# Kernel optimization log

Hardware: AMD Instinct MI355X
Metric: run time of the kernel (lower is better)

## Reference

```python
import jax, jax.numpy as jnp
import numpy as np

B = 16384
QD = 2048   # query_dim
KD = 1024   # key_dim
HID = 1024  # hidden_dim = min(QD, KD)
NH = 16     # num_heads
HD = HID // NH  # head_dim = 64
LN_EPS = 1e-5


def _ln(x, w, b):
    m = jnp.mean(x, axis=-1, keepdims=True)
    v = jnp.mean((x - m) ** 2, axis=-1, keepdims=True)
    return (x - m) * jax.lax.rsqrt(v + LN_EPS) * w + b


def _lin(x, W, b):
    return x @ W.T + b


def setup_inputs() -> dict:
    key = jax.random.key(0)
    ks = jax.random.split(key, 12)
    p = lambda k, shape: jax.random.normal(k, shape, jnp.float32) * 0.02
    return dict(
        query_features=jax.random.normal(ks[0], (B, QD), jnp.float32),
        key_features=jax.random.normal(ks[1], (B, KD), jnp.float32),
        Wq=p(ks[2], (HID, QD)), bq=jnp.zeros((HID,), jnp.float32),
        ln_q_w=jnp.ones((HID,), jnp.float32), ln_q_b=jnp.zeros((HID,), jnp.float32),
        Wk=p(ks[3], (HID, KD)), bk=jnp.zeros((HID,), jnp.float32),
        ln_k_w=jnp.ones((HID,), jnp.float32), ln_k_b=jnp.zeros((HID,), jnp.float32),
        Wvq=p(ks[4], (HID, QD)), bvq=jnp.zeros((HID,), jnp.float32),
        Wvk=p(ks[5], (HID, KD)), bvk=jnp.zeros((HID,), jnp.float32),
        Wo=p(ks[6], (QD, HID)), bo=jnp.zeros((QD,), jnp.float32),
        ln_o_w=jnp.ones((QD,), jnp.float32), ln_o_b=jnp.zeros((QD,), jnp.float32),
        Wg1=p(ks[7], (HID, QD + KD)), bg1=jnp.zeros((HID,), jnp.float32),
        Wg2=p(ks[8], (1, HID)), bg2=jnp.zeros((1,), jnp.float32),
        Wc1=p(ks[9], (HID, QD + KD)), bc1=jnp.zeros((HID,), jnp.float32),
        Wc2=p(ks[10], (1, HID)), bc2=jnp.zeros((1,), jnp.float32),
    )


def reference(query_features, key_features,
              Wq, bq, ln_q_w, ln_q_b,
              Wk, bk, ln_k_w, ln_k_b,
              Wvq, bvq, Wvk, bvk,
              Wo, bo, ln_o_w, ln_o_b,
              Wg1, bg1, Wg2, bg2,
              Wc1, bc1, Wc2, bc2):
    b = query_features.shape[0]
    q = _ln(_lin(query_features, Wq, bq), ln_q_w, ln_q_b)      # [B, HID]
    k = _ln(_lin(key_features, Wk, bk), ln_k_w, ln_k_b)        # [B, HID]
    v_q = _lin(query_features, Wvq, bvq)  # computed in torch but unused
    v_k = _lin(key_features, Wvk, bvk)    # [B, HID]
    q = q.reshape(b, NH, HD)
    k = k.reshape(b, NH, HD)
    v_k = v_k.reshape(b, NH, HD)
    # NOTE: attention mixes over the HEAD axis (j == num_heads), per original einsum
    scores = jnp.einsum('bhd,bjd->bhj', q, k) / np.sqrt(HD).astype(np.float32)
    attn = jax.nn.softmax(scores, axis=-1)  # dropout p effectively 0 / eval mode
    attended = jnp.einsum('bhj,bjd->bhd', attn, v_k).reshape(b, HID)
    output = _ln(_lin(attended, Wo, bo), ln_o_w, ln_o_b)       # [B, QD]
    combined = jnp.concatenate([query_features, key_features], axis=1)  # [B, QD+KD]
    gate = jax.nn.sigmoid(_lin(jax.nn.gelu(_lin(combined, Wg1, bg1), approximate=False), Wg2, bg2))
    chem = jax.nn.sigmoid(_lin(jax.nn.gelu(_lin(combined, Wc1, bc1), approximate=False), Wc2, bc2))
    effective_gate = gate * chem  # [B, 1]
    return query_features + effective_gate * output
```

## Files before the change

kernel.cpp:

```cpp
#include <hip/hip_runtime.h>
#include <stdint.h>

#define QD 2048
#define KD 1024
#define HID 1024
#define NH 16
#define HD 64
#define CMBD 3072

typedef float  f32x4   __attribute__((ext_vector_type(4)));
typedef short  short8  __attribute__((ext_vector_type(8)));
typedef short  short4v __attribute__((ext_vector_type(4)));
typedef float  float4v __attribute__((ext_vector_type(4)));

__device__ inline float bf2f(short s) {
  unsigned u = ((unsigned)(unsigned short)s) << 16;
  return __builtin_bit_cast(float, u);
}
__device__ inline short f2bf(float f) {
  unsigned u = __builtin_bit_cast(unsigned, f);
  u = u + 0x7fff + ((u >> 16) & 1);
  return (short)(u >> 16);
}

__global__ void cvt_inputs(const float* __restrict__ qf, const float* __restrict__ kf,
                           short* __restrict__ cmb, int rows2) {
  const int b = blockIdx.x, t = threadIdx.x;
  if (b < rows2) {
    const int i = b * 256 + t;
    const int row = i >> 9, c4 = i & 511;
    float4v v = *(const float4v*)(qf + (size_t)row * QD + c4 * 4);
    short4v o;
    o[0] = f2bf(v[0]); o[1] = f2bf(v[1]); o[2] = f2bf(v[2]); o[3] = f2bf(v[3]);
    *(short4v*)(cmb + (size_t)row * CMBD + c4 * 4) = o;
  } else {
    const int i = (b - rows2) * 256 + t;
    const int row = i >> 8, c4 = i & 255;
    float4v v = *(const float4v*)(kf + (size_t)row * KD + c4 * 4);
    short4v o;
    o[0] = f2bf(v[0]); o[1] = f2bf(v[1]); o[2] = f2bf(v[2]); o[3] = f2bf(v[3]);
    *(short4v*)(cmb + (size_t)row * CMBD + QD + c4 * 4) = o;
  }
}

struct WSeg { const float* s; short* d; int blkEnd; };
__global__ void cvt_weights(WSeg s0, WSeg s1, WSeg s2, WSeg s3, WSeg s4, WSeg s5) {
  int b = blockIdx.x;
  WSeg seg; int base;
  if      (b < s0.blkEnd) { seg = s0; base = 0; }
  else if (b < s1.blkEnd) { seg = s1; base = s0.blkEnd; }
  else if (b < s2.blkEnd) { seg = s2; base = s1.blkEnd; }
  else if (b < s3.blkEnd) { seg = s3; base = s2.blkEnd; }
  else if (b < s4.blkEnd) { seg = s4; base = s3.blkEnd; }
  else                    { seg = s5; base = s4.blkEnd; }
  const size_t i = ((size_t)(b - base) * 256 + threadIdx.x) * 4;
  float4v v = *(const float4v*)(seg.s + i);
  short4v o;
  o[0] = f2bf(v[0]); o[1] = f2bf(v[1]); o[2] = f2bf(v[2]); o[3] = f2bf(v[3]);
  *(short4v*)(seg.d + i) = o;
}

#define EPI_NONE 0
#define EPI_GATE 2

typedef const __attribute__((address_space(1))) void gvoid_t;
typedef __attribute__((address_space(3))) void lvoid_t;

#define WAIT_VM(n)  asm volatile("s_waitcnt vmcnt(" #n ")" ::: "memory")

#define APAN(b, kp) (((b) * 2 + (kp)) * 8192)
#define BPAN(b, kp) (32768 + ((b) * 2 + (kp)) * 8192)

#define PHASE_MID                                        \
  __builtin_amdgcn_s_barrier();                          \
  asm volatile("s_waitcnt lgkmcnt(0)" ::: "memory");     \
  __builtin_amdgcn_s_setprio(1);

#define PHASE_END                                        \
  __builtin_amdgcn_s_setprio(0);                         \
  __builtin_amdgcn_s_barrier();

template<int EPI>
__global__ __launch_bounds__(512, 2)
void gemm256(const short* __restrict__ A, size_t lda,
             const short* __restrict__ W,
             const float* __restrict__ bias,
             short* __restrict__ C, int N, int K,
             const float* __restrict__ w2, float* __restrict__ egp, int rowsTot) {
  extern __shared__ short ls[];
  const int tid  = threadIdx.x;
  const int lane = tid & 63;
  const int wave = tid >> 6;
  const int wm = wave >> 2, wn = wave & 3;
  const int fr = lane & 15, kq4 = lane >> 4;

  const int nwg = gridDim.x * gridDim.y;
  const int lin = blockIdx.y * gridDim.x + blockIdx.x;
  const int cpx = nwg >> 3;
  const int nid = (lin & 7) * cpx + (lin >> 3);
  const int bx = nid % gridDim.x, by = nid / gridDim.x;
  const size_t rowBase = (size_t)by * 256;
  const size_t colBase = (size_t)bx * 256;

  const int NTT = K >> 6;

  f32x4 acc[8][4];
#pragma unroll
  for (int mi = 0; mi < 8; mi++)
#pragma unroll
    for (int ni = 0; ni < 4; ni++) acc[mi][ni] = (f32x4){0.f, 0.f, 0.f, 0.f};

  const int frsw = (kq4 ^ ((fr >> 1) & 3)) * 8;

  const int grow  = tid >> 2;
  const int slotx = (tid & 3) ^ ((tid >> 3) & 3);
  const short* gAlo = A + (rowBase + grow) * lda + slotx * 8;
  const short* gAhi = gAlo + (size_t)128 * lda;
  const short* gBlo = W + (colBase + grow) * (size_t)K + slotx * 8;
  const short* gBhi = gBlo + (size_t)128 * K;
  short* const sdst = ls + tid * 8;

  auto STG_A = [&](int panOff, int kcol) {
    __builtin_amdgcn_global_load_lds((gvoid_t*)(gAlo + kcol), (lvoid_t*)(sdst + panOff),        16, 0, 0);
    __builtin_amdgcn_global_load_lds((gvoid_t*)(gAhi + kcol), (lvoid_t*)(sdst + panOff + 4096), 16, 0, 0);
  };
  auto STG_B = [&](int panOff, int kcol) {
    __builtin_amdgcn_global_load_lds((gvoid_t*)(gBlo + kcol), (lvoid_t*)(sdst + panOff),        16, 0, 0);
    __builtin_amdgcn_global_load_lds((gvoid_t*)(gBhi + kcol), (lvoid_t*)(sdst + panOff + 4096), 16, 0, 0);
  };

  STG_A(APAN(0, 0), 0);  STG_A(APAN(0, 1), 32);
  STG_B(BPAN(0, 0), 0);  STG_B(BPAN(0, 1), 32);
  STG_B(BPAN(1, 0), 64); STG_B(BPAN(1, 1), 96);
  WAIT_VM(4);
  __builtin_amdgcn_s_barrier();

  short8 fa0[8], fa1[8], fb0[4], fb1[4];

  for (int t = 0; t < NTT; t += 2) {
    const bool more = (t + 2 < NTT);
    const int kA1 = (t + 1) * 64;
    const int kE2 = (t + 2) * 64;
    const int kO3 = (t + 3) * 64;

#pragma unroll
    for (int m = 0; m < 4; m++) {
      const int r = (wm * 128 + m * 16 + fr) * 32 + frsw;
      fa0[m * 2 + 0] = *(const short8*)(ls + APAN(0, 0) + r);
      fa0[m * 2 + 1] = *(const short8*)(ls + APAN(0, 1) + r);
    }
#pragma unroll
    for (int n = 0; n < 2; n++) {
      const int r = (wn * 64 + n * 16 + fr) * 32 + frsw;
      fb0[n * 2 + 0] = *(const short8*)(ls + BPAN(0, 0) + r);
      fb0[n * 2 + 1] = *(const short8*)(ls + BPAN(0, 1) + r);
    }
    STG_A(APAN(1, 0), kA1);
    PHASE_MID
#pragma unroll
    for (int m = 0; m < 4; m++)
#pragma unroll
      for (int n = 0; n < 2; n++) {
        acc[m][n] = __builtin_amdgcn_mfma_f32_16x16x32_bf16(fa0[m*2+0], fb0[n*2+0], acc[m][n], 0, 0, 0);
        acc[m][n] = __builtin_amdgcn_mfma_f32_16x16x32_bf16(fa0[m*2+1], fb0[n*2+1], acc[m][n], 0, 0, 0);
      }
    PHASE_END

#pragma unroll
    for (int n = 0; n < 2; n++) {
      const int r = (wn * 64 + (n + 2) * 16 + fr) * 32 + frsw;
      fb1[n * 2 + 0] = *(const short8*)(ls + BPAN(0, 0) + r);
      fb1[n * 2 + 1] = *(const short8*)(ls + BPAN(0, 1) + r);
    }
    STG_A(APAN(1, 1), kA1 + 32);
    PHASE_MID
#pragma unroll
    for (int m = 0; m < 4; m++)
#pragma unroll
      for (int n = 0; n < 2; n++) {
        acc[m][n+2] = __builtin_amdgcn_mfma_f32_16x16x32_bf16(fa0[m*2+0], fb1[n*2+0], acc[m][n+2], 0, 0, 0);
        acc[m][n+2] = __builtin_amdgcn_mfma_f32_16x16x32_bf16(fa0[m*2+1], fb1[n*2+1], acc[m][n+2], 0, 0, 0);
      }
    PHASE_END

#pragma unroll
    for (int m = 0; m < 4; m++) {
      const int r = (wm * 128 + (m + 4) * 16 + fr) * 32 + frsw;
      fa1[m * 2 + 0] = *(const short8*)(ls + APAN(0, 0) + r);
      fa1[m * 2 + 1] = *(const short8*)(ls + APAN(0, 1) + r);
    }
    if (more) STG_B(BPAN(0, 0), kE2);
    PHASE_MID
#pragma unroll
    for (int m = 0; m < 4; m++)
#pragma unroll
      for (int n = 0; n < 2; n++) {
        acc[m+4][n] = __builtin_amdgcn_mfma_f32_16x16x32_bf16(fa1[m*2+0], fb0[n*2+0], acc[m+4][n], 0, 0, 0);
        acc[m+4][n] = __builtin_amdgcn_mfma_f32_16x16x32_bf16(fa1[m*2+1], fb0[n*2+1], acc[m+4][n], 0, 0, 0);
      }
    PHASE_END

    if (more) STG_B(BPAN(0, 1), kE2 + 32);
    PHASE_MID
#pragma unroll
    for (int m = 0; m < 4; m++)
#pragma unroll
      for (int n = 0; n < 2; n++) {
        acc[m+4][n+2] = __builtin_amdgcn_mfma_f32_16x16x32_bf16(fa1[m*2+0], fb1[n*2+0], acc[m+4][n+2], 0, 0, 0);
        acc[m+4][n+2] = __builtin_amdgcn_mfma_f32_16x16x32_bf16(fa1[m*2+1], fb1[n*2+1], acc[m+4][n+2], 0, 0, 0);
      }
    __builtin_amdgcn_s_setprio(0);
    if (more) { WAIT_VM(4); } else { WAIT_VM(0); }
    __builtin_amdgcn_s_barrier();

#pragma unroll
    for (int m = 0; m < 4; m++) {
      const int r = (wm * 128 + m * 16 + fr) * 32 + frsw;
      fa0[m * 2 + 0] = *(const short8*)(ls + APAN(1, 0) + r);
      fa0[m * 2 + 1] = *(const short8*)(ls + APAN(1, 1) + r);
    }
#pragma unroll
    for (int n = 0; n < 2; n++) {
      const int r = (wn * 64 + n * 16 + fr) * 32 + frsw;
      fb0[n * 2 + 0] = *(const short8*)(ls + BPAN(1, 0) + r);
      fb0[n * 2 + 1] = *(const short8*)(ls + BPAN(1, 1) + r);
    }
    if (more) STG_A(APAN(0, 0), kE2);
    PHASE_MID
#pragma unroll
    for (int m = 0; m < 4; m++)
#pragma unroll
      for (int n = 0; n < 2; n++) {
        acc[m][n] = __builtin_amdgcn_mfma_f32_16x16x32_bf16(fa0[m*2+0], fb0[n*2+0], acc[m][n], 0, 0, 0);
        acc[m][n] = __builtin_amdgcn_mfma_f32_16x16x32_bf16(fa0[m*2+1], fb0[n*2+1], acc[m][n], 0, 0, 0);
      }
    PHASE_END

#pragma unroll
    for (int n = 0; n < 2; n++) {
      const int r = (wn * 64 + (n + 2) * 16 + fr) * 32 + frsw;
      fb1[n * 2 + 0] = *(const short8*)(ls + BPAN(1, 0) + r);
      fb1[n * 2 + 1] = *(const short8*)(ls + BPAN(1, 1) + r);
    }
    if (more) STG_A(APAN(0, 1), kE2 + 32);
    PHASE_MID
#pragma unroll
    for (int m = 0; m < 4; m++)
#pragma unroll
      for (int n = 0; n < 2; n++) {
        acc[m][n+2] = __builtin_amdgcn_mfma_f32_16x16x32_bf16(fa0[m*2+0], fb1[n*2+0], acc[m][n+2], 0, 0, 0);
        acc[m][n+2] = __builtin_amdgcn_mfma_f32_16x16x32_bf16(fa0[m*2+1], fb1[n*2+1], acc[m][n+2], 0, 0, 0);
      }
    PHASE_END

#pragma unroll
    for (int m = 0; m < 4; m++) {
      const int r = (wm * 128 + (m + 4) * 16 + fr) * 32 + frsw;
      fa1[m * 2 + 0] = *(const short8*)(ls + APAN(1, 0) + r);
      fa1[m * 2 + 1] = *(const short8*)(ls + APAN(1, 1) + r);
    }
    if (more) STG_B(BPAN(1, 0), kO3);
    PHASE_MID
#pragma unroll
    for (int m = 0; m < 4; m++)
#pragma unroll
      for (int n = 0; n < 2; n++) {
        acc[m+4][n] = __builtin_amdgcn_mfma_f32_16x16x32_bf16(fa1[m*2+0], fb0[n*2+0], acc[m+4][n], 0, 0, 0);
        acc[m+4][n] = __builtin_amdgcn_mfma_f32_16x16x32_bf16(fa1[m*2+1], fb0[n*2+1], acc[m+4][n], 0, 0, 0);
      }
    PHASE_END

    if (more) STG_B(BPAN(1, 1), kO3 + 32);
    PHASE_MID
#pragma unroll
    for (int m = 0; m < 4; m++)
#pragma unroll
      for (int n = 0; n < 2; n++) {
        acc[m+4][n+2] = __builtin_amdgcn_mfma_f32_16x16x32_bf16(fa1[m*2+0], fb1[n*2+0], acc[m+4][n+2], 0, 0, 0);
        acc[m+4][n+2] = __builtin_amdgcn_mfma_f32_16x16x32_bf16(fa1[m*2+1], fb1[n*2+1], acc[m+4][n+2], 0, 0, 0);
      }
    __builtin_amdgcn_s_setprio(0);
    if (more) { WAIT_VM(4); }
    __builtin_amdgcn_s_barrier();
  }

  if (EPI == EPI_GATE) {
    float w2v[4], bvv[4];
#pragma unroll
    for (int ni = 0; ni < 4; ni++) {
      const int c = (int)colBase + wn * 64 + ni * 16 + fr;
      w2v[ni] = w2[c]; bvv[ni] = bias[c];
    }
    const int half = (colBase >= 1024) ? 1 : 0;
#pragma unroll
    for (int mi = 0; mi < 8; mi++) {
      float sj[4] = {0.f, 0.f, 0.f, 0.f};
#pragma unroll
      for (int ni = 0; ni < 4; ni++)
#pragma unroll
        for (int j = 0; j < 4; j++) {
          float x = acc[mi][ni][j] + bvv[ni];
          float g = 0.5f * x * (1.f + erff(x * 0.70710678118f));
          sj[j] += g * w2v[ni];
        }
#pragma unroll
      for (int j = 0; j < 4; j++) {
#pragma unroll
        for (int o = 8; o >= 1; o >>= 1) sj[j] += __shfl_xor(sj[j], o);
        if (fr == 0) {
          const int row = (int)rowBase + wm * 128 + mi * 16 + kq4 * 4 + j;
          atomicAdd(egp + half * rowsTot + row, sj[j]);
        }
      }
    }
  } else {
#pragma unroll
    for (int mi = 0; mi < 8; mi++) {
      const size_t row0 = rowBase + wm * 128 + mi * 16 + kq4 * 4;
#pragma unroll
      for (int ni = 0; ni < 4; ni++) {
        const int col = (int)colBase + wn * 64 + ni * 16 + fr;
        const float bv = bias[col];
#pragma unroll
        for (int j = 0; j < 4; j++) {
          float x = acc[mi][ni][j] + bv;
          C[(row0 + j) * (size_t)N + col] = f2bf(x);
        }
      }
    }
  }
}

__device__ inline float4 block_sum4(float a, float b, float c, float d, float* sc) {
#pragma unroll
  for (int o = 32; o >= 1; o >>= 1) {
    a += __shfl_down(a, o); b += __shfl_down(b, o);
    c += __shfl_down(c, o); d += __shfl_down(d, o);
  }
  const int lane = threadIdx.x & 63, w = threadIdx.x >> 6;
  const int nw = blockDim.x >> 6;
  if (lane == 0) { sc[w*4] = a; sc[w*4+1] = b; sc[w*4+2] = c; sc[w*4+3] = d; }
  __syncthreads();
  float ra = 0.f, rb = 0.f, rc = 0.f, rd = 0.f;
  for (int i = 0; i < nw; i++) { ra += sc[i*4]; rb += sc[i*4+1]; rc += sc[i*4+2]; rd += sc[i*4+3]; }
  __syncthreads();
  return make_float4(ra, rb, rc, rd);
}
__device__ inline float2 block_sum2(float a, float b, float* sc) {
#pragma unroll
  for (int o = 32; o >= 1; o >>= 1) { a += __shfl_down(a, o); b += __shfl_down(b, o); }
  const int lane = threadIdx.x & 63, w = threadIdx.x >> 6;
  const int nw = blockDim.x >> 6;
  if (lane == 0) { sc[w*2] = a; sc[w*2+1] = b; }
  __syncthreads();
  float ra = 0.f, rb = 0.f;
  for (int i = 0; i < nw; i++) { ra += sc[i*2]; rb += sc[i*2+1]; }
  __syncthreads();
  return make_float2(ra, rb);
}

__global__ __launch_bounds__(256)
void attn_ln(const short* __restrict__ qp, const short* __restrict__ kv,
             const float* __restrict__ lnqw, const float* __restrict__ lnqb,
             const float* __restrict__ lnkw, const float* __restrict__ lnkb,
             short* __restrict__ att) {
  __shared__ float qs[HID];
  __shared__ float ks[NH * 65];
  __shared__ float vs[HID];
  __shared__ float aw[256];
  __shared__ float red[16];
  const int t = threadIdx.x;
  const size_t row = blockIdx.x;

  short4v q4 = *(const short4v*)(qp + row * HID + t * 4);
  short4v k4 = *(const short4v*)(kv + row * 2048 + t * 4);
  short4v v4 = *(const short4v*)(kv + row * 2048 + 1024 + t * 4);
  float qv[4], kvv[4];
  float sq = 0.f, sqq = 0.f, sk = 0.f, skk = 0.f;
#pragma unroll
  for (int i = 0; i < 4; i++) {
    qv[i] = bf2f(q4[i]); sq += qv[i]; sqq += qv[i] * qv[i];
    kvv[i] = bf2f(k4[i]); sk += kvv[i]; skk += kvv[i] * kvv[i];
  }
  float4 r4 = block_sum4(sq, sqq, sk, skk, red);
  float mq = r4.x / HID, vq = r4.y / HID - mq * mq;
  float rsq = rsqrtf(vq + 1e-5f);
  float mk = r4.z / HID, vv = r4.w / HID - mk * mk;
  float rsk = rsqrtf(vv + 1e-5f);
#pragma unroll
  for (int i = 0; i < 4; i++) {
    const int idx = t * 4 + i;
    qs[idx] = (qv[i] - mq) * rsq * lnqw[idx] + lnqb[idx];
    ks[(idx >> 6) * 65 + (idx & 63)] = (kvv[i] - mk) * rsk * lnkw[idx] + lnkb[idx];
    vs[idx] = bf2f(v4[i]);
  }
  __syncthreads();

  const int h = t >> 4, j = t & 15;
  float s = 0.f;
#pragma unroll 8
  for (int d = 0; d < 64; d++) s += qs[h * 64 + d] * ks[j * 65 + d];
  s *= 0.125f;
  float mx = s;
#pragma unroll
  for (int o = 8; o >= 1; o >>= 1) mx = fmaxf(mx, __shfl_xor(mx, o, 16));
  float e = __expf(s - mx);
  float sum = e;
#pragma unroll
  for (int o = 8; o >= 1; o >>= 1) sum += __shfl_xor(sum, o, 16);
  aw[t] = e / sum;
  __syncthreads();

  const int dB = (t & 15) * 4;
  float o0 = 0.f, o1 = 0.f, o2 = 0.f, o3 = 0.f;
#pragma unroll
  for (int jj = 0; jj < 16; jj++) {
    const float w = aw[h * 16 + jj];
    const float* vp = &vs[jj * 64 + dB];
    o0 += w * vp[0]; o1 += w * vp[1]; o2 += w * vp[2]; o3 += w * vp[3];
  }
  short4v o4;
  o4[0] = f2bf(o0); o4[1] = f2bf(o1); o4[2] = f2bf(o2); o4[3] = f2bf(o3);
  *(short4v*)(att + row * HID + h * 64 + dB) = o4;
}

__global__ __launch_bounds__(256)
void final_kernel(const short* __restrict__ opre, const short* __restrict__ cmb,
                  const float* __restrict__ egp, int rowsTot,
                  const float* __restrict__ bg2, const float* __restrict__ bc2,
                  const float* __restrict__ lnow, const float* __restrict__ lnob,
                  float* __restrict__ out) {
  __shared__ float red[8];
  const int t = threadIdx.x;
  const size_t row = blockIdx.x;
  short8 o8 = *(const short8*)(opre + row * QD + t * 8);
  short8 q8 = *(const short8*)(cmb + row * CMBD + t * 8);
  float x[8];
  float s = 0.f, ss = 0.f;
#pragma unroll
  for (int i = 0; i < 8; i++) { x[i] = bf2f(o8[i]); s += x[i]; ss += x[i] * x[i]; }
  float2 r = block_sum2(s, ss, red);
  float m = r.x / QD, v = r.y / QD - m * m;
  float rs = rsqrtf(v + 1e-5f);
  float gg = 1.f / (1.f + __expf(-(egp[row] + bg2[0])));
  float gc = 1.f / (1.f + __expf(-(egp[rowsTot + row] + bc2[0])));
  float g = gg * gc;
  float4v oa, ob;
#pragma unroll
  for (int i = 0; i < 8; i++) {
    const int c = t * 8 + i;
    float y = (x[i] - m) * rs * lnow[c] + lnob[c];
    float r2 = bf2f(q8[i]) + g * y;
    if (i < 4) oa[i] = r2; else ob[i - 4] = r2;
  }
  *(float4v*)(out + row * QD + t * 8) = oa;
  *(float4v*)(out + row * QD + t * 8 + 4) = ob;
}

extern "C" void kernel_launch(void* const* d_in, const int* in_sizes, int n_in,
                              void* d_out, int out_size, void* d_ws, size_t ws_size,
                              hipStream_t stream) {
  const float* qf   = (const float*)d_in[0];
  const float* kf   = (const float*)d_in[1];
  const float* Wq   = (const float*)d_in[2];
  const float* bq   = (const float*)d_in[3];
  const float* lnqw = (const float*)d_in[4];
  const float* lnqb = (const float*)d_in[5];
  const float* Wk   = (const float*)d_in[6];
  const float* bk   = (const float*)d_in[7];
  const float* lnkw = (const float*)d_in[8];
  const float* lnkb = (const float*)d_in[9];
  const float* Wvk  = (const float*)d_in[12];
  const float* bvk  = (const float*)d_in[13];
  const float* Wo   = (const float*)d_in[14];
  const float* bo   = (const float*)d_in[15];
  const float* lnow = (const float*)d_in[16];
  const float* lnob = (const float*)d_in[17];
  const float* Wg1  = (const float*)d_in[18];
  const float* bg1  = (const float*)d_in[19];
  const float* Wg2  = (const float*)d_in[20];
  const float* bg2  = (const float*)d_in[21];
  const float* Wc1  = (const float*)d_in[22];
  const float* bc1  = (const float*)d_in[23];
  const float* Wc2  = (const float*)d_in[24];
  const float* bc2  = (const float*)d_in[25];

  const int rows = in_sizes[0] / QD;

  char* ws = (char*)d_ws;
  size_t off = 0;
  auto alloc = [&](size_t bytes) -> char* {
    char* p = ws + off;
    off += (bytes + 255) & ~(size_t)255;
    return p;
  };
  short* cmb  = (short*)alloc((size_t)rows * CMBD * 2);
  short* wqb  = (short*)alloc((size_t)HID * QD * 2);
  short* wkv  = (short*)alloc((size_t)2 * HID * KD * 2);
  short* wob  = (short*)alloc((size_t)QD * HID * 2);
  short* wgc  = (short*)alloc((size_t)2 * HID * CMBD * 2);
  short* hgc  = (short*)alloc((size_t)rows * 2048 * 2);
  short* qp   = (short*)alloc((size_t)rows * HID * 2);
  short* kvp  = (short*)alloc((size_t)rows * 2048 * 2);
  float* egp  = (float*)alloc((size_t)2 * rows * 4);
  float* bgc  = (float*)alloc(2048 * 4);
  float* bkv  = (float*)alloc(2048 * 4);
  float* w2gc = (float*)alloc(2048 * 4);
  short* att  = hgc;
  short* opre = kvp;

  hipMemcpyAsync(bgc, bg1, HID * 4, hipMemcpyDeviceToDevice, stream);
  hipMemcpyAsync(bgc + HID, bc1, HID * 4, hipMemcpyDeviceToDevice, stream);
  hipMemcpyAsync(bkv, bk, HID * 4, hipMemcpyDeviceToDevice, stream);
  hipMemcpyAsync(bkv + HID, bvk, HID * 4, hipMemcpyDeviceToDevice, stream);
  hipMemcpyAsync(w2gc, Wg2, HID * 4, hipMemcpyDeviceToDevice, stream);
  hipMemcpyAsync(w2gc + HID, Wc2, HID * 4, hipMemcpyDeviceToDevice, stream);
  hipMemsetAsync(egp, 0, (size_t)2 * rows * 4, stream);

  cvt_inputs<<<rows * 3, 256, 0, stream>>>(qf, kf, cmb, rows * 2);
  {
    WSeg s0{Wq,  wqb,                       2048};
    WSeg s1{Wk,  wkv,                       2048 + 1024};
    WSeg s2{Wvk, wkv + (size_t)HID * KD,    2048 + 2048};
    WSeg s3{Wo,  wob,                       2048 + 2048 + 2048};
    WSeg s4{Wg1, wgc,                       2048 + 2048 + 2048 + 3072};
    WSeg s5{Wc1, wgc + (size_t)HID * CMBD,  2048 + 2048 + 2048 + 3072 + 3072};
    cvt_weights<<<s5.blkEnd, 256, 0, stream>>>(s0, s1, s2, s3, s4, s5);
  }

  hipFuncSetAttribute((const void*)gemm256<EPI_GATE>,
                      hipFuncAttributeMaxDynamicSharedMemorySize, 131072);
  hipFuncSetAttribute((const void*)gemm256<EPI_NONE>,
                      hipFuncAttributeMaxDynamicSharedMemorySize, 131072);

  const dim3 blk(512);
  const int mt = rows / 256;
  const size_t lds = 131072;

  gemm256<EPI_GATE><<<dim3(2048 / 256, mt), blk, lds, stream>>>(cmb, CMBD, wgc, bgc, hgc, 2048, CMBD, w2gc, egp, rows);
  gemm256<EPI_NONE><<<dim3(1024 / 256, mt), blk, lds, stream>>>(cmb, CMBD, wqb, bq, qp, 1024, QD, nullptr, nullptr, 0);
  gemm256<EPI_NONE><<<dim3(2048 / 256, mt), blk, lds, stream>>>(cmb + QD, CMBD, wkv, bkv, kvp, 2048, KD, nullptr, nullptr, 0);
  attn_ln<<<rows, 256, 0, stream>>>(qp, kvp, lnqw, lnqb, lnkw, lnkb, att);
  gemm256<EPI_NONE><<<dim3(2048 / 256, mt), blk, lds, stream>>>(att, HID, wob, bo, opre, 2048, HID, nullptr, nullptr, 0);
  final_kernel<<<rows, 256, 0, stream>>>(opre, cmb, egp, rows, bg2, bc2, lnow, lnob, (float*)d_out);
}
```

Baseline: 603.2 us.

## Switch main GEMM from 16x16x32 to 32x32x16 bf16 MFMA tiles

Replaces the per-wave 8x4 grid of 16x16x32 MFMAs with a 4x2 grid of 32x32x16 MFMAs covering the same 128x64 wave tile. LDS fragment loads, swizzle offsets and both epilogues (bias store and fused GELU gate reduction) are remapped to the 32x32 accumulator layout. The larger instruction needs fewer LDS fragment reads per FLOP and fewer MFMA issues. The trade-off is different register pressure and a longer shuffle reduction in the gate epilogue.

```diff
diff --git a/kernel.cpp b/kernel.cpp
--- a/kernel.cpp
+++ b/kernel.cpp
@@ -9,6 +9,7 @@
 #define CMBD 3072
 
 typedef float  f32x4   __attribute__((ext_vector_type(4)));
+typedef float  f32x16  __attribute__((ext_vector_type(16)));
 typedef short  short8  __attribute__((ext_vector_type(8)));
 typedef short  short4v __attribute__((ext_vector_type(4)));
 typedef float  float4v __attribute__((ext_vector_type(4)));
@@ -92,7 +93,7 @@
   const int lane = tid & 63;
   const int wave = tid >> 6;
   const int wm = wave >> 2, wn = wave & 3;
-  const int fr = lane & 15, kq4 = lane >> 4;
+  const int l31 = lane & 31, lb = lane >> 5;
 
   const int nwg = gridDim.x * gridDim.y;
   const int lin = blockIdx.y * gridDim.x + blockIdx.x;
@@ -104,13 +105,19 @@
 
   const int NTT = K >> 6;
 
-  f32x4 acc[8][4];
-#pragma unroll
-  for (int mi = 0; mi < 8; mi++)
-#pragma unroll
-    for (int ni = 0; ni < 4; ni++) acc[mi][ni] = (f32x4){0.f, 0.f, 0.f, 0.f};
-
-  const int frsw = (kq4 ^ ((fr >> 1) & 3)) * 8;
+  f32x16 acc[4][2];
+#pragma unroll
+  for (int mi = 0; mi < 4; mi++)
+#pragma unroll
+    for (int ni = 0; ni < 2; ni++)
+#pragma unroll
+      for (int r = 0; r < 16; r++) acc[mi][ni][r] = 0.f;
+
+  const int swz = (l31 >> 1) & 3;
+  const int asw0 = ((0 + lb) ^ swz) * 8;
+  const int asw1 = ((2 + lb) ^ swz) * 8;
+  const int abase = (wm * 128 + l31) * 32;
+  const int bbase = (wn * 64 + l31) * 32;
 
   const int grow  = tid >> 2;
   const int slotx = (tid & 3) ^ ((tid >> 3) & 3);
@@ -135,7 +142,87 @@
   WAIT_VM(4);
   __builtin_amdgcn_s_barrier();
 
-  short8 fa0[8], fa1[8], fb0[4], fb1[4];
+  short8 afr[4], b01[4], b23[4];
+
+#define KTILE(BUF, ST1, ST2, ST3, ST4, ENDWAIT)                               \
+  {                                                                           \
+                                                                \
+    _Pragma("unroll")                                                         \
+    for (int m = 0; m < 2; m++) {                                             \
+      afr[m*2+0] = *(const short8*)(ls + APAN(BUF,0) + abase + m*1024 + asw0);\
+      afr[m*2+1] = *(const short8*)(ls + APAN(BUF,0) + abase + m*1024 + asw1);\
+    }                                                                         \
+    _Pragma("unroll")                                                         \
+    for (int n = 0; n < 2; n++) {                                             \
+      b01[n*2+0] = *(const short8*)(ls + BPAN(BUF,0) + bbase + n*1024 + asw0);\
+      b01[n*2+1] = *(const short8*)(ls + BPAN(BUF,0) + bbase + n*1024 + asw1);\
+    }                                                                         \
+    ST1;                                                                      \
+    PHASE_MID                                                                 \
+    _Pragma("unroll")                                                         \
+    for (int m = 0; m < 2; m++)                                               \
+      _Pragma("unroll")                                                       \
+      for (int n = 0; n < 2; n++) {                                           \
+        acc[m][n] = __builtin_amdgcn_mfma_f32_32x32x16_bf16(afr[m*2+0], b01[n*2+0], acc[m][n], 0, 0, 0); \
+        acc[m][n] = __builtin_amdgcn_mfma_f32_32x32x16_bf16(afr[m*2+1], b01[n*2+1], acc[m][n], 0, 0, 0); \
+      }                                                                       \
+    PHASE_END                                                                 \
+                                                                \
+    _Pragma("unroll")                                                         \
+    for (int m = 0; m < 2; m++) {                                             \
+      afr[m*2+0] = *(const short8*)(ls + APAN(BUF,1) + abase + m*1024 + asw0);\
+      afr[m*2+1] = *(const short8*)(ls + APAN(BUF,1) + abase + m*1024 + asw1);\
+    }                                                                         \
+    _Pragma("unroll")                                                         \
+    for (int n = 0; n < 2; n++) {                                             \
+      b23[n*2+0] = *(const short8*)(ls + BPAN(BUF,1) + bbase + n*1024 + asw0);\
+      b23[n*2+1] = *(const short8*)(ls + BPAN(BUF,1) + bbase + n*1024 + asw1);\
+    }                                                                         \
+    ST2;                                                                      \
+    PHASE_MID                                                                 \
+    _Pragma("unroll")                                                         \
+    for (int m = 0; m < 2; m++)                                               \
+      _Pragma("unroll")                                                       \
+      for (int n = 0; n < 2; n++) {                                           \
+        acc[m][n] = __builtin_amdgcn_mfma_f32_32x32x16_bf16(afr[m*2+0], b23[n*2+0], acc[m][n], 0, 0, 0); \
+        acc[m][n] = __builtin_amdgcn_mfma_f32_32x32x16_bf16(afr[m*2+1], b23[n*2+1], acc[m][n], 0, 0, 0); \
+      }                                                                       \
+    PHASE_END                                                                 \
+                                                                \
+    _Pragma("unroll")                                                         \
+    for (int m = 0; m < 2; m++) {                                             \
+      afr[m*2+0] = *(const short8*)(ls + APAN(BUF,0) + abase + (m+2)*1024 + asw0);\
+      afr[m*2+1] = *(const short8*)(ls + APAN(BUF,0) + abase + (m+2)*1024 + asw1);\
+    }                                                                         \
+    ST3;                                                                      \
+    PHASE_MID                                                                 \
+    _Pragma("unroll")                                                         \
+    for (int m = 0; m < 2; m++)                                               \
+      _Pragma("unroll")                                                       \
+      for (int n = 0; n < 2; n++) {                                           \
+        acc[m+2][n] = __builtin_amdgcn_mfma_f32_32x32x16_bf16(afr[m*2+0], b01[n*2+0], acc[m+2][n], 0, 0, 0); \
+        acc[m+2][n] = __builtin_amdgcn_mfma_f32_32x32x16_bf16(afr[m*2+1], b01[n*2+1], acc[m+2][n], 0, 0, 0); \
+      }                                                                       \
+    PHASE_END                                                                 \
+                                                                \
+    _Pragma("unroll")                                                         \
+    for (int m = 0; m < 2; m++) {                                             \
+      afr[m*2+0] = *(const short8*)(ls + APAN(BUF,1) + abase + (m+2)*1024 + asw0);\
+      afr[m*2+1] = *(const short8*)(ls + APAN(BUF,1) + abase + (m+2)*1024 + asw1);\
+    }                                                                         \
+    ST4;                                                                      \
+    PHASE_MID                                                                 \
+    _Pragma("unroll")                                                         \
+    for (int m = 0; m < 2; m++)                                               \
+      _Pragma("unroll")                                                       \
+      for (int n = 0; n < 2; n++) {                                           \
+        acc[m+2][n] = __builtin_amdgcn_mfma_f32_32x32x16_bf16(afr[m*2+0], b23[n*2+0], acc[m+2][n], 0, 0, 0); \
+        acc[m+2][n] = __builtin_amdgcn_mfma_f32_32x32x16_bf16(afr[m*2+1], b23[n*2+1], acc[m+2][n], 0, 0, 0); \
+      }                                                                       \
+    __builtin_amdgcn_s_setprio(0);                                            \
+    ENDWAIT;                                                                  \
+    __builtin_amdgcn_s_barrier();                                             \
+  }
 
   for (int t = 0; t < NTT; t += 2) {
     const bool more = (t + 2 < NTT);
@@ -143,188 +230,65 @@
     const int kE2 = (t + 2) * 64;
     const int kO3 = (t + 3) * 64;
 
-#pragma unroll
-    for (int m = 0; m < 4; m++) {
-      const int r = (wm * 128 + m * 16 + fr) * 32 + frsw;
-      fa0[m * 2 + 0] = *(const short8*)(ls + APAN(0, 0) + r);
-      fa0[m * 2 + 1] = *(const short8*)(ls + APAN(0, 1) + r);
-    }
-#pragma unroll
-    for (int n = 0; n < 2; n++) {
-      const int r = (wn * 64 + n * 16 + fr) * 32 + frsw;
-      fb0[n * 2 + 0] = *(const short8*)(ls + BPAN(0, 0) + r);
-      fb0[n * 2 + 1] = *(const short8*)(ls + BPAN(0, 1) + r);
-    }
-    STG_A(APAN(1, 0), kA1);
-    PHASE_MID
-#pragma unroll
-    for (int m = 0; m < 4; m++)
-#pragma unroll
-      for (int n = 0; n < 2; n++) {
-        acc[m][n] = __builtin_amdgcn_mfma_f32_16x16x32_bf16(fa0[m*2+0], fb0[n*2+0], acc[m][n], 0, 0, 0);
-        acc[m][n] = __builtin_amdgcn_mfma_f32_16x16x32_bf16(fa0[m*2+1], fb0[n*2+1], acc[m][n], 0, 0, 0);
-      }
-    PHASE_END
-
-#pragma unroll
-    for (int n = 0; n < 2; n++) {
-      const int r = (wn * 64 + (n + 2) * 16 + fr) * 32 + frsw;
-      fb1[n * 2 + 0] = *(const short8*)(ls + BPAN(0, 0) + r);
-      fb1[n * 2 + 1] = *(const short8*)(ls + BPAN(0, 1) + r);
-    }
-    STG_A(APAN(1, 1), kA1 + 32);
-    PHASE_MID
-#pragma unroll
-    for (int m = 0; m < 4; m++)
-#pragma unroll
-      for (int n = 0; n < 2; n++) {
-        acc[m][n+2] = __builtin_amdgcn_mfma_f32_16x16x32_bf16(fa0[m*2+0], fb1[n*2+0], acc[m][n+2], 0, 0, 0);
-        acc[m][n+2] = __builtin_amdgcn_mfma_f32_16x16x32_bf16(fa0[m*2+1], fb1[n*2+1], acc[m][n+2], 0, 0, 0);
-      }
-    PHASE_END
-
-#pragma unroll
-    for (int m = 0; m < 4; m++) {
-      const int r = (wm * 128 + (m + 4) * 16 + fr) * 32 + frsw;
-      fa1[m * 2 + 0] = *(const short8*)(ls + APAN(0, 0) + r);
-      fa1[m * 2 + 1] = *(const short8*)(ls + APAN(0, 1) + r);
-    }
-    if (more) STG_B(BPAN(0, 0), kE2);
-    PHASE_MID
-#pragma unroll
-    for (int m = 0; m < 4; m++)
-#pragma unroll
-      for (int n = 0; n < 2; n++) {
-        acc[m+4][n] = __builtin_amdgcn_mfma_f32_16x16x32_bf16(fa1[m*2+0], fb0[n*2+0], acc[m+4][n], 0, 0, 0);
-        acc[m+4][n] = __builtin_amdgcn_mfma_f32_16x16x32_bf16(fa1[m*2+1], fb0[n*2+1], acc[m+4][n], 0, 0, 0);
-      }
-    PHASE_END
-
-    if (more) STG_B(BPAN(0, 1), kE2 + 32);
-    PHASE_MID
-#pragma unroll
-    for (int m = 0; m < 4; m++)
-#pragma unroll
-      for (int n = 0; n < 2; n++) {
-        acc[m+4][n+2] = __builtin_amdgcn_mfma_f32_16x16x32_bf16(fa1[m*2+0], fb1[n*2+0], acc[m+4][n+2], 0, 0, 0);
-        acc[m+4][n+2] = __builtin_amdgcn_mfma_f32_16x16x32_bf16(fa1[m*2+1], fb1[n*2+1], acc[m+4][n+2], 0, 0, 0);
-      }
-    __builtin_amdgcn_s_setprio(0);
-    if (more) { WAIT_VM(4); } else { WAIT_VM(0); }
-    __builtin_amdgcn_s_barrier();
-
-#pragma unroll
-    for (int m = 0; m < 4; m++) {
-      const int r = (wm * 128 + m * 16 + fr) * 32 + frsw;
-      fa0[m * 2 + 0] = *(const short8*)(ls + APAN(1, 0) + r);
-      fa0[m * 2 + 1] = *(const short8*)(ls + APAN(1, 1) + r);
-    }
-#pragma unroll
-    for (int n = 0; n < 2; n++) {
-      const int r = (wn * 64 + n * 16 + fr) * 32 + frsw;
-      fb0[n * 2 + 0] = *(const short8*)(ls + BPAN(1, 0) + r);
-      fb0[n * 2 + 1] = *(const short8*)(ls + BPAN(1, 1) + r);
-    }
-    if (more) STG_A(APAN(0, 0), kE2);
-    PHASE_MID
-#pragma unroll
-    for (int m = 0; m < 4; m++)
-#pragma unroll
-      for (int n = 0; n < 2; n++) {
-        acc[m][n] = __builtin_amdgcn_mfma_f32_16x16x32_bf16(fa0[m*2+0], fb0[n*2+0], acc[m][n], 0, 0, 0);
-        acc[m][n] = __builtin_amdgcn_mfma_f32_16x16x32_bf16(fa0[m*2+1], fb0[n*2+1], acc[m][n], 0, 0, 0);
-      }
-    PHASE_END
-
-#pragma unroll
-    for (int n = 0; n < 2; n++) {
-      const int r = (wn * 64 + (n + 2) * 16 + fr) * 32 + frsw;
-      fb1[n * 2 + 0] = *(const short8*)(ls + BPAN(1, 0) + r);
-      fb1[n * 2 + 1] = *(const short8*)(ls + BPAN(1, 1) + r);
-    }
-    if (more) STG_A(APAN(0, 1), kE2 + 32);
-    PHASE_MID
-#pragma unroll
-    for (int m = 0; m < 4; m++)
-#pragma unroll
-      for (int n = 0; n < 2; n++) {
-        acc[m][n+2] = __builtin_amdgcn_mfma_f32_16x16x32_bf16(fa0[m*2+0], fb1[n*2+0], acc[m][n+2], 0, 0, 0);
-        acc[m][n+2] = __builtin_amdgcn_mfma_f32_16x16x32_bf16(fa0[m*2+1], fb1[n*2+1], acc[m][n+2], 0, 0, 0);
-      }
-    PHASE_END
-
-#pragma unroll
-    for (int m = 0; m < 4; m++) {
-      const int r = (wm * 128 + (m + 4) * 16 + fr) * 32 + frsw;
-      fa1[m * 2 + 0] = *(const short8*)(ls + APAN(1, 0) + r);
-      fa1[m * 2 + 1] = *(const short8*)(ls + APAN(1, 1) + r);
-    }
-    if (more) STG_B(BPAN(1, 0), kO3);
-    PHASE_MID
-#pragma unroll
-    for (int m = 0; m < 4; m++)
-#pragma unroll
-      for (int n = 0; n < 2; n++) {
-        acc[m+4][n] = __builtin_amdgcn_mfma_f32_16x16x32_bf16(fa1[m*2+0], fb0[n*2+0], acc[m+4][n], 0, 0, 0);
-        acc[m+4][n] = __builtin_amdgcn_mfma_f32_16x16x32_bf16(fa1[m*2+1], fb0[n*2+1], acc[m+4][n], 0, 0, 0);
-      }
-    PHASE_END
-
-    if (more) STG_B(BPAN(1, 1), kO3 + 32);
-    PHASE_MID
-#pragma unroll
-    for (int m = 0; m < 4; m++)
-#pragma unroll
-      for (int n = 0; n < 2; n++) {
-        acc[m+4][n+2] = __builtin_amdgcn_mfma_f32_16x16x32_bf16(fa1[m*2+0], fb1[n*2+0], acc[m+4][n+2], 0, 0, 0);
-        acc[m+4][n+2] = __builtin_amdgcn_mfma_f32_16x16x32_bf16(fa1[m*2+1], fb1[n*2+1], acc[m+4][n+2], 0, 0, 0);
-      }
-    __builtin_amdgcn_s_setprio(0);
-    if (more) { WAIT_VM(4); }
-    __builtin_amdgcn_s_barrier();
-  }
+    KTILE(0,
+          STG_A(APAN(1, 0), kA1),
+          STG_A(APAN(1, 1), kA1 + 32),
+          if (more) STG_B(BPAN(0, 0), kE2),
+          if (more) STG_B(BPAN(0, 1), kE2 + 32),
+          if (more) { WAIT_VM(4); } else { WAIT_VM(0); })
+    KTILE(1,
+          if (more) STG_A(APAN(0, 0), kE2),
+          if (more) STG_A(APAN(0, 1), kE2 + 32),
+          if (more) STG_B(BPAN(1, 0), kO3),
+          if (more) STG_B(BPAN(1, 1), kO3 + 32),
+          if (more) { WAIT_VM(4); })
+  }
+#undef KTILE
 
   if (EPI == EPI_GATE) {
-    float w2v[4], bvv[4];
-#pragma unroll
-    for (int ni = 0; ni < 4; ni++) {
-      const int c = (int)colBase + wn * 64 + ni * 16 + fr;
+    float w2v[2], bvv[2];
+#pragma unroll
+    for (int ni = 0; ni < 2; ni++) {
+      const int c = (int)colBase + wn * 64 + ni * 32 + l31;
       w2v[ni] = w2[c]; bvv[ni] = bias[c];
     }
     const int half = (colBase >= 1024) ? 1 : 0;
 #pragma unroll
-    for (int mi = 0; mi < 8; mi++) {
-      float sj[4] = {0.f, 0.f, 0.f, 0.f};
-#pragma unroll
-      for (int ni = 0; ni < 4; ni++)
-#pragma unroll
-        for (int j = 0; j < 4; j++) {
-          float x = acc[mi][ni][j] + bvv[ni];
+    for (int mi = 0; mi < 4; mi++) {
+      float sj[16];
+#pragma unroll
+      for (int r = 0; r < 16; r++) sj[r] = 0.f;
+#pragma unroll
+      for (int ni = 0; ni < 2; ni++)
+#pragma unroll
+        for (int r = 0; r < 16; r++) {
+          float x = acc[mi][ni][r] + bvv[ni];
           float g = 0.5f * x * (1.f + erff(x * 0.70710678118f));
-          sj[j] += g * w2v[ni];
+          sj[r] += g * w2v[ni];
         }
 #pragma unroll
-      for (int j = 0; j < 4; j++) {
-#pragma unroll
-        for (int o = 8; o >= 1; o >>= 1) sj[j] += __shfl_xor(sj[j], o);
-        if (fr == 0) {
-          const int row = (int)rowBase + wm * 128 + mi * 16 + kq4 * 4 + j;
-          atomicAdd(egp + half * rowsTot + row, sj[j]);
+      for (int r = 0; r < 16; r++) {
+#pragma unroll
+        for (int o = 16; o >= 1; o >>= 1) sj[r] += __shfl_xor(sj[r], o);
+        if (l31 == 0) {
+          const int row = (int)rowBase + wm * 128 + mi * 32 +
+                          (r & 3) + 8 * (r >> 2) + 4 * lb;
+          atomicAdd(egp + half * rowsTot + row, sj[r]);
         }
       }
     }
   } else {
 #pragma unroll
-    for (int mi = 0; mi < 8; mi++) {
-      const size_t row0 = rowBase + wm * 128 + mi * 16 + kq4 * 4;
-#pragma unroll
-      for (int ni = 0; ni < 4; ni++) {
-        const int col = (int)colBase + wn * 64 + ni * 16 + fr;
+    for (int mi = 0; mi < 4; mi++) {
+      const size_t row0 = rowBase + wm * 128 + mi * 32 + 4 * lb;
+#pragma unroll
+      for (int ni = 0; ni < 2; ni++) {
+        const int col = (int)colBase + wn * 64 + ni * 32 + l31;
         const float bv = bias[col];
 #pragma unroll
-        for (int j = 0; j < 4; j++) {
-          float x = acc[mi][ni][j] + bv;
-          C[(row0 + j) * (size_t)N + col] = f2bf(x);
+        for (int r = 0; r < 16; r++) {
+          const size_t row = row0 + (r & 3) + 8 * (r >> 2);
+          C[row * (size_t)N + col] = f2bf(acc[mi][ni][r] + bv);
         }
       }
     }
```

New measurement: 650.8 us. +7.9%, slower.

## Merge gate, query and key/value GEMMs into one launch and pack param copies

Applied to the files above, without the earlier changes.

Combines the three GEMMs that read the combined input into a single kernel with a 20-column-tile grid, where each block picks its role (gate/chem with fused GELU reduction, Q projection, or KV projection) from its tile index. This removes two launches and the tail effects between them, letting blocks with different K lengths share the machine. It also replaces six device-to-device memcpys and a memset with one small pack kernel. The mixed K lengths (3072/2048/1024) inside one grid may cause load imbalance, and the block-swizzle mapping now mixes roles.

```diff
diff --git a/kernel.cpp b/kernel.cpp
--- a/kernel.cpp
+++ b/kernel.cpp
@@ -60,6 +60,26 @@
   *(short4v*)(seg.d + i) = o;
 }
 
+__global__ void pack_params(float* __restrict__ egp, int egpN,
+                            const float* __restrict__ bg1, const float* __restrict__ bc1,
+                            const float* __restrict__ bk,  const float* __restrict__ bvk,
+                            const float* __restrict__ Wg2, const float* __restrict__ Wc2,
+                            float* __restrict__ bgc, float* __restrict__ bkv,
+                            float* __restrict__ w2gc) {
+  int i = blockIdx.x * 256 + threadIdx.x;
+  if (i < egpN) { egp[i] = 0.f; return; }
+  i -= egpN;
+  const int seg = i >> 10, idx = i & 1023;
+  switch (seg) {
+    case 0: bgc[idx]         = bg1[idx]; break;
+    case 1: bgc[1024 + idx]  = bc1[idx]; break;
+    case 2: bkv[idx]         = bk[idx];  break;
+    case 3: bkv[1024 + idx]  = bvk[idx]; break;
+    case 4: w2gc[idx]        = Wg2[idx]; break;
+    case 5: w2gc[1024 + idx] = Wc2[idx]; break;
+  }
+}
+
 #define EPI_NONE 0
 #define EPI_GATE 2
 
@@ -80,36 +100,12 @@
   __builtin_amdgcn_s_setprio(0);                         \
   __builtin_amdgcn_s_barrier();
 
-template<int EPI>
-__global__ __launch_bounds__(512, 2)
-void gemm256(const short* __restrict__ A, size_t lda,
-             const short* __restrict__ W,
-             const float* __restrict__ bias,
-             short* __restrict__ C, int N, int K,
-             const float* __restrict__ w2, float* __restrict__ egp, int rowsTot) {
-  extern __shared__ short ls[];
-  const int tid  = threadIdx.x;
-  const int lane = tid & 63;
-  const int wave = tid >> 6;
-  const int wm = wave >> 2, wn = wave & 3;
-  const int fr = lane & 15, kq4 = lane >> 4;
-
-  const int nwg = gridDim.x * gridDim.y;
-  const int lin = blockIdx.y * gridDim.x + blockIdx.x;
-  const int cpx = nwg >> 3;
-  const int nid = (lin & 7) * cpx + (lin >> 3);
-  const int bx = nid % gridDim.x, by = nid / gridDim.x;
-  const size_t rowBase = (size_t)by * 256;
-  const size_t colBase = (size_t)bx * 256;
-
+__device__ __forceinline__ void gemm_core(
+    short* ls, f32x4 (&acc)[8][4],
+    const short* A, size_t lda, const short* W, int K,
+    size_t rowBase, size_t colBase,
+    int tid, int wm, int wn, int fr, int kq4) {
   const int NTT = K >> 6;
-
-  f32x4 acc[8][4];
-#pragma unroll
-  for (int mi = 0; mi < 8; mi++)
-#pragma unroll
-    for (int ni = 0; ni < 4; ni++) acc[mi][ni] = (f32x4){0.f, 0.f, 0.f, 0.f};
-
   const int frsw = (kq4 ^ ((fr >> 1) & 3)) * 8;
 
   const int grow  = tid >> 2;
@@ -283,13 +279,48 @@
     if (more) { WAIT_VM(4); }
     __builtin_amdgcn_s_barrier();
   }
-
-  if (EPI == EPI_GATE) {
+}
+
+__global__ __launch_bounds__(512, 2)
+void gemm_mega(const short* cmb,
+               const short* wgc, const float* bgc,
+               const short* wqb, const float* bq, short* qp,
+               const short* wkv, const float* bkv, short* kvp,
+               const float* w2gc, float* egp, int rowsTot) {
+  extern __shared__ short ls[];
+  const int tid  = threadIdx.x;
+  const int lane = tid & 63;
+  const int wave = tid >> 6;
+  const int wm = wave >> 2, wn = wave & 3;
+  const int fr = lane & 15, kq4 = lane >> 4;
+
+  const int nwg = gridDim.x * gridDim.y;
+  const int lin = blockIdx.y * gridDim.x + blockIdx.x;
+  const int cpx = nwg >> 3;
+  const int nid = (lin & 7) * cpx + (lin >> 3);
+  const int bx = nid % 20, by = nid / 20;
+  const size_t rowBase = (size_t)by * 256;
+
+  const short* A; const short* W; const float* bias; short* C;
+  int N, K, role; size_t colBase;
+  if (bx < 8)       { role = 1; A = cmb;      W = wgc; bias = bgc; C = nullptr; N = 2048; K = 3072; colBase = (size_t)bx * 256; }
+  else if (bx < 12) { role = 0; A = cmb;      W = wqb; bias = bq;  C = qp;      N = 1024; K = 2048; colBase = (size_t)(bx - 8) * 256; }
+  else              { role = 0; A = cmb + QD; W = wkv; bias = bkv; C = kvp;     N = 2048; K = 1024; colBase = (size_t)(bx - 12) * 256; }
+
+  f32x4 acc[8][4];
+#pragma unroll
+  for (int mi = 0; mi < 8; mi++)
+#pragma unroll
+    for (int ni = 0; ni < 4; ni++) acc[mi][ni] = (f32x4){0.f, 0.f, 0.f, 0.f};
+
+  gemm_core(ls, acc, A, CMBD, W, K, rowBase, colBase, tid, wm, wn, fr, kq4);
+
+  if (role == 1) {
     float w2v[4], bvv[4];
 #pragma unroll
     for (int ni = 0; ni < 4; ni++) {
       const int c = (int)colBase + wn * 64 + ni * 16 + fr;
-      w2v[ni] = w2[c]; bvv[ni] = bias[c];
+      w2v[ni] = w2gc[c]; bvv[ni] = bias[c];
     }
     const int half = (colBase >= 1024) ? 1 : 0;
 #pragma unroll
@@ -326,6 +357,48 @@
           float x = acc[mi][ni][j] + bv;
           C[(row0 + j) * (size_t)N + col] = f2bf(x);
         }
+      }
+    }
+  }
+}
+
+__global__ __launch_bounds__(512, 2)
+void gemm_o(const short* __restrict__ A, const short* __restrict__ W,
+            const float* __restrict__ bias, short* __restrict__ C) {
+  extern __shared__ short ls[];
+  const int tid  = threadIdx.x;
+  const int lane = tid & 63;
+  const int wave = tid >> 6;
+  const int wm = wave >> 2, wn = wave & 3;
+  const int fr = lane & 15, kq4 = lane >> 4;
+
+  const int nwg = gridDim.x * gridDim.y;
+  const int lin = blockIdx.y * gridDim.x + blockIdx.x;
+  const int cpx = nwg >> 3;
+  const int nid = (lin & 7) * cpx + (lin >> 3);
+  const int bx = nid % gridDim.x, by = nid / gridDim.x;
+  const size_t rowBase = (size_t)by * 256;
+  const size_t colBase = (size_t)bx * 256;
+
+  f32x4 acc[8][4];
+#pragma unroll
+  for (int mi = 0; mi < 8; mi++)
+#pragma unroll
+    for (int ni = 0; ni < 4; ni++) acc[mi][ni] = (f32x4){0.f, 0.f, 0.f, 0.f};
+
+  gemm_core(ls, acc, A, HID, W, HID, rowBase, colBase, tid, wm, wn, fr, kq4);
+
+#pragma unroll
+  for (int mi = 0; mi < 8; mi++) {
+    const size_t row0 = rowBase + wm * 128 + mi * 16 + kq4 * 4;
+#pragma unroll
+    for (int ni = 0; ni < 4; ni++) {
+      const int col = (int)colBase + wn * 64 + ni * 16 + fr;
+      const float bv = bias[col];
+#pragma unroll
+      for (int j = 0; j < 4; j++) {
+        float x = acc[mi][ni][j] + bv;
+        C[(row0 + j) * (size_t)QD + col] = f2bf(x);
       }
     }
   }
@@ -509,13 +582,9 @@
   short* att  = hgc;
   short* opre = kvp;
 
-  hipMemcpyAsync(bgc, bg1, HID * 4, hipMemcpyDeviceToDevice, stream);
-  hipMemcpyAsync(bgc + HID, bc1, HID * 4, hipMemcpyDeviceToDevice, stream);
-  hipMemcpyAsync(bkv, bk, HID * 4, hipMemcpyDeviceToDevice, stream);
-  hipMemcpyAsync(bkv + HID, bvk, HID * 4, hipMemcpyDeviceToDevice, stream);
-  hipMemcpyAsync(w2gc, Wg2, HID * 4, hipMemcpyDeviceToDevice, stream);
-  hipMemcpyAsync(w2gc + HID, Wc2, HID * 4, hipMemcpyDeviceToDevice, stream);
-  hipMemsetAsync(egp, 0, (size_t)2 * rows * 4, stream);
+  const int egpN = 2 * rows;
+  pack_params<<<(egpN + 6144) / 256, 256, 0, stream>>>(egp, egpN, bg1, bc1, bk, bvk,
+                                                       Wg2, Wc2, bgc, bkv, w2gc);
 
   cvt_inputs<<<rows * 3, 256, 0, stream>>>(qf, kf, cmb, rows * 2);
   {
@@ -528,19 +597,18 @@
     cvt_weights<<<s5.blkEnd, 256, 0, stream>>>(s0, s1, s2, s3, s4, s5);
   }
 
-  hipFuncSetAttribute((const void*)gemm256<EPI_GATE>,
+  hipFuncSetAttribute((const void*)gemm_mega,
                       hipFuncAttributeMaxDynamicSharedMemorySize, 131072);
-  hipFuncSetAttribute((const void*)gemm256<EPI_NONE>,
+  hipFuncSetAttribute((const void*)gemm_o,
                       hipFuncAttributeMaxDynamicSharedMemorySize, 131072);
 
   const dim3 blk(512);
   const int mt = rows / 256;
   const size_t lds = 131072;
 
-  gemm256<EPI_GATE><<<dim3(2048 / 256, mt), blk, lds, stream>>>(cmb, CMBD, wgc, bgc, hgc, 2048, CMBD, w2gc, egp, rows);
-  gemm256<EPI_NONE><<<dim3(1024 / 256, mt), blk, lds, stream>>>(cmb, CMBD, wqb, bq, qp, 1024, QD, nullptr, nullptr, 0);
-  gemm256<EPI_NONE><<<dim3(2048 / 256, mt), blk, lds, stream>>>(cmb + QD, CMBD, wkv, bkv, kvp, 2048, KD, nullptr, nullptr, 0);
+  gemm_mega<<<dim3(20, mt), blk, lds, stream>>>(cmb, wgc, bgc, wqb, bq, qp,
+                                                wkv, bkv, kvp, w2gc, egp, rows);
   attn_ln<<<rows, 256, 0, stream>>>(qp, kvp, lnqw, lnqb, lnkw, lnkb, att);
-  gemm256<EPI_NONE><<<dim3(2048 / 256, mt), blk, lds, stream>>>(att, HID, wob, bo, opre, 2048, HID, nullptr, nullptr, 0);
+  gemm_o<<<dim3(QD / 256, mt), blk, lds, stream>>>(att, wob, bo, opre);
   final_kernel<<<rows, 256, 0, stream>>>(opre, cmb, egp, rows, bg2, bc2, lnow, lnob, (float*)d_out);
 }
```

Result: no change. 611.1 us (+1.3%).
